# Kernel tuning notes

Measured on AMD Instinct MI355X. Metric: run time of the kernel, lower is better.

Reference implementation:

```python
import jax, jax.numpy as jnp
import numpy as np

# UKF constants (Merwe scaled sigma points)
ALPHA, BETA, KAPPA = 1.0, 2.0, 0.0
JITTER = 1e-4
S_DIM, C_DIM, M_DIM, H_DIM = 8, 2, 4, 32


def setup_inputs() -> dict:
    B, T = 1024, 256
    key = jax.random.key(0)
    ks = jax.random.split(key, 11)
    inp = {
        "X0": 0.1 * jax.random.normal(ks[0], (B, S_DIM), dtype=jnp.float32),
        "u": jax.random.normal(ks[1], (B, T, C_DIM), dtype=jnp.float32),
        "y": jax.random.normal(ks[2], (B, T, M_DIM), dtype=jnp.float32),
        # learned process model f(x,u) = x + tanh([x;u] W1 + b1) W2 + b2
        "W1": 0.1 * jax.random.normal(ks[3], (S_DIM + C_DIM, H_DIM), dtype=jnp.float32),
        "b1": jnp.zeros((H_DIM,), dtype=jnp.float32),
        "W2": 0.1 * jax.random.normal(ks[4], (H_DIM, S_DIM), dtype=jnp.float32),
        "b2": jnp.zeros((S_DIM,), dtype=jnp.float32),
        # linear measurement model h(x) = Hm x
        "Hm": 0.3 * jax.random.normal(ks[5], (M_DIM, S_DIM), dtype=jnp.float32),
        # learned diagonal noise / initial covariance (softplus parameterized)
        "lq": -3.0 + 0.1 * jax.random.normal(ks[6], (S_DIM,), dtype=jnp.float32),
        "lr": -2.0 + 0.1 * jax.random.normal(ks[7], (M_DIM,), dtype=jnp.float32),
        "lp0": -1.0 + 0.1 * jax.random.normal(ks[8], (S_DIM,), dtype=jnp.float32),
    }
    return inp


def reference(X0, u, y, W1, b1, W2, b2, Hm, lq, lr, lp0):
    B, n = X0.shape
    T = u.shape[1]
    lam = ALPHA ** 2 * (n + KAPPA) - n
    c = n + lam
    Wm = jnp.concatenate([jnp.array([lam / c], dtype=X0.dtype),
                          jnp.full((2 * n,), 0.5 / c, dtype=X0.dtype)])
    Wc = Wm.at[0].add(1.0 - ALPHA ** 2 + BETA)
    I = jnp.eye(n, dtype=X0.dtype)

    Q = jnp.diag(jax.nn.softplus(lq))            # [n,n] process noise
    R = jnp.diag(jax.nn.softplus(lr))            # [m,m] measurement noise
    P0 = jnp.broadcast_to(jnp.diag(jax.nn.softplus(lp0)), (B, n, n))  # P0(X0)

    def f(pts, u_t):  # pts [B,2n+1,n], u_t [B,C]
        uu = jnp.broadcast_to(u_t[:, None, :], pts.shape[:2] + (u_t.shape[-1],))
        z = jnp.concatenate([pts, uu], axis=-1)
        return pts + jnp.tanh(z @ W1 + b1) @ W2 + b2

    def step(carry, inp_t):
        x, P = carry            # x [B,n], P [B,n,n]
        u_t, y_t = inp_t        # u at i-1, y at i
        # sigma points via Cholesky of scaled covariance
        L = jnp.linalg.cholesky(c * P + JITTER * I)
        offs = jnp.swapaxes(L, -1, -2)  # [B,n,n]: row i = i-th column of L
        pts = jnp.concatenate([x[:, None], x[:, None] + offs, x[:, None] - offs], axis=1)  # [B,2n+1,n]
        # predict
        pts_f = f(pts, u_t)
        x_pred = jnp.einsum('s,bsn->bn', Wm, pts_f)
        dx = pts_f - x_pred[:, None]
        P_pred = jnp.einsum('s,bsn,bsm->bnm', Wc, dx, dx) + Q
        P_pred = 0.5 * (P_pred + jnp.swapaxes(P_pred, -1, -2)) + JITTER * I
        # measurement update (linear h reused on propagated sigma points)
        y_pts = pts_f @ Hm.T
        y_pred = jnp.einsum('s,bsm->bm', Wm, y_pts)
        dy = y_pts - y_pred[:, None]
        Sy = jnp.einsum('s,bsi,bsj->bij', Wc, dy, dy) + R
        Sy = 0.5 * (Sy + jnp.swapaxes(Sy, -1, -2))
        Pxy = jnp.einsum('s,bsn,bsm->bnm', Wc, dx, dy)
        # K = Pxy Sy^{-1} via solve on Sy (SPD)
        K = jnp.swapaxes(jnp.linalg.solve(Sy, jnp.swapaxes(Pxy, -1, -2)), -1, -2)
        x_new = x_pred + jnp.einsum('bnm,bm->bn', K, y_t - y_pred)
        P_new = P_pred - K @ Sy @ jnp.swapaxes(K, -1, -2)
        P_new = 0.5 * (P_new + jnp.swapaxes(P_new, -1, -2)) + JITTER * I
        q_e = 0.5 * jnp.linalg.slogdet(P_pred)[1]  # [B]
        r_e = 0.5 * jnp.linalg.slogdet(Sy)[1]      # [B]
        return (x_new, P_new), (x_new, P_new, q_e, r_e)

    # steps i = 1..T-1 use u[:, i-1] and y[:, i]
    u_seq = jnp.swapaxes(u[:, :T - 1], 0, 1)  # [T-1,B,C]
    y_seq = jnp.swapaxes(y[:, 1:], 0, 1)      # [T-1,B,M]
    _, (Xs, Ps, qs, rs) = jax.lax.scan(step, (X0, P0), (u_seq, y_seq))

    X = jnp.concatenate([X0[:, None], jnp.swapaxes(Xs, 0, 1)], axis=1)        # [B,T,n]
    P = jnp.concatenate([P0[:, None], jnp.swapaxes(Ps, 0, 1)], axis=1)        # [B,T,n,n]
    zcol = jnp.zeros((X0.shape[0], 1), dtype=X0.dtype)
    q_entr = jnp.concatenate([zcol, jnp.swapaxes(qs, 0, 1)], axis=1)          # [B,T]
    r_entr = jnp.concatenate([zcol, jnp.swapaxes(rs, 0, 1)], axis=1)          # [B,T]
    return X, P, q_entr, r_entr
```

## Files before the change

kernel.cpp:

```cpp
#include <hip/hip_runtime.h>
#include <math.h>

#define B_LEN 1024
#define T_LEN 256
#define HST 36

__device__ __forceinline__ float fast_rcp(float x) { return __builtin_amdgcn_rcpf(x); }
__device__ __forceinline__ float fast_rsq(float x) { return __builtin_amdgcn_rsqf(x); }
__device__ __forceinline__ float lane_bcast(float v, int l) {
    return __int_as_float(__builtin_amdgcn_readlane(__float_as_int(v), l));
}
__device__ __forceinline__ float fast_tanh(float x) {
    float e = __expf(2.0f * x);
    return 1.0f - 2.0f * fast_rcp(e + 1.0f);
}
__device__ __forceinline__ float softplus_f(float x) {
    return (x > 20.0f) ? x : log1pf(expf(x));
}

__global__ __launch_bounds__(128, 2)
void ukf_kernel(const float* __restrict__ X0, const float* __restrict__ U,
                const float* __restrict__ Y,  const float* __restrict__ W1,
                const float* __restrict__ B1, const float* __restrict__ W2,
                const float* __restrict__ B2, const float* __restrict__ HM,
                const float* __restrict__ LQ, const float* __restrict__ LR,
                const float* __restrict__ LP0, float* __restrict__ out)
{
    const int tid  = threadIdx.x;
    const int wid  = tid >> 6;
    const int lane = tid & 63;
    const int b    = blockIdx.x;
    const int k8   = lane & 7;
    const int g8   = lane >> 3;
    const int i8   = g8;
    const int j8   = k8;
    const int h32  = lane & 31;
    const int p2   = lane >> 5;
    const int m4   = lane & 3;
    const int sy   = lane >> 2;

    __shared__ __align__(16) float u_sh[T_LEN * 2];
    __shared__ __align__(16) float y_sh[T_LEN * 4];
    __shared__ __align__(16) float pts_sh[17 * 8];
    __shared__ __align__(16) float hid_sh[17 * HST];
    __shared__ __align__(16) float pf_sh[17 * 8];
    __shared__ __align__(16) float dx_sh[17 * 8];
    __shared__ __align__(16) float yp_sh[17 * 4];
    __shared__ __align__(16) float xp_sh[8];
    __shared__ __align__(16) float ypred_sh[4];
    __shared__ __align__(16) float Sy_sh[16];
    __shared__ __align__(16) float Pxy_sh[32];
    __shared__ __align__(16) float K_sh[32];
    __shared__ __align__(16) float Pp_sh[64];

    for (int k = tid; k < T_LEN * 2; k += 128) u_sh[k] = U[(size_t)b * (T_LEN * 2) + k];
    for (int k = tid; k < T_LEN * 4; k += 128) y_sh[k] = Y[(size_t)b * (T_LEN * 4) + k];

    float w1r[10];
    #pragma unroll
    for (int d = 0; d < 10; ++d) w1r[d] = W1[d * 32 + h32];
    const float b1r = B1[h32];
    float w2r[32];
    #pragma unroll
    for (int h = 0; h < 32; ++h) w2r[h] = W2[h * 8 + k8];
    const float b2r = B2[k8];
    float hmr[8];
    #pragma unroll
    for (int d = 0; d < 8; ++d) hmr[d] = HM[m4 * 8 + d];

    const float qdiag = softplus_f(LQ[i8]);
    const float rdiag = softplus_f(LR[m4]);

    const size_t Xbase = (size_t)b * T_LEN * 8;
    const size_t Pbase = (size_t)B_LEN * T_LEN * 8  + (size_t)b * T_LEN * 64;
    const size_t qbase = (size_t)B_LEN * T_LEN * 72 + (size_t)b * T_LEN;
    const size_t rbase = (size_t)B_LEN * T_LEN * 73 + (size_t)b * T_LEN;

    float xn[8], Pc[8];
    {
        const float4 xa = *(const float4*)&X0[b * 8];
        const float4 xb = *(const float4*)&X0[b * 8 + 4];
        xn[0] = xa.x; xn[1] = xa.y; xn[2] = xa.z; xn[3] = xa.w;
        xn[4] = xb.x; xn[5] = xb.y; xn[6] = xb.z; xn[7] = xb.w;
        const float p0k = softplus_f(LP0[k8]);
        #pragma unroll
        for (int i = 0; i < 8; ++i) Pc[i] = (i == k8) ? p0k : 0.0f;
    }
    if (wid == 0) {
        if (g8 == 0) {
            #pragma unroll
            for (int i = 0; i < 8; ++i) out[Pbase + i * 8 + k8] = Pc[i];
        }
        if (lane == 0) {
            *(float4*)&out[Xbase]     = make_float4(xn[0], xn[1], xn[2], xn[3]);
            *(float4*)&out[Xbase + 4] = make_float4(xn[4], xn[5], xn[6], xn[7]);
            out[qbase] = 0.0f; out[rbase] = 0.0f;
        }
    }

    for (int t = 1; t < T_LEN; ++t) {
        if (wid == 0) {
            float a[8];
            #pragma unroll
            for (int i = 0; i < 8; ++i) a[i] = 8.0f * Pc[i] + ((i == k8) ? 1e-4f : 0.0f);
            #pragma unroll
            for (int j = 0; j < 8; ++j) {
                const float dj  = lane_bcast(a[j], j);
                const float rv  = fast_rsq(dj);
                const float rv2 = rv * rv;
                float u[8];
                #pragma unroll
                for (int i = j + 1; i < 8; ++i) u[i] = lane_bcast(a[i], j);
                if (k8 == j) {
                    a[j] = dj * rv;
                    #pragma unroll
                    for (int i = j + 1; i < 8; ++i) a[i] *= rv;
                } else if (k8 > j) {
                    const float tt = a[j] * rv2;
                    #pragma unroll
                    for (int i = j + 1; i < 8; ++i) a[i] = fmaf(-tt, u[i], a[i]);
                }
            }
            float Lc[8];
            #pragma unroll
            for (int i = 0; i < 8; ++i) Lc[i] = (i >= k8) ? a[i] : 0.0f;
            if (g8 == 0) {
                *(float4*)&pts_sh[(1 + k8) * 8] =
                    make_float4(xn[0] + Lc[0], xn[1] + Lc[1], xn[2] + Lc[2], xn[3] + Lc[3]);
                *(float4*)&pts_sh[(1 + k8) * 8 + 4] =
                    make_float4(xn[4] + Lc[4], xn[5] + Lc[5], xn[6] + Lc[6], xn[7] + Lc[7]);
            } else if (g8 == 1) {
                *(float4*)&pts_sh[(9 + k8) * 8] =
                    make_float4(xn[0] - Lc[0], xn[1] - Lc[1], xn[2] - Lc[2], xn[3] - Lc[3]);
                *(float4*)&pts_sh[(9 + k8) * 8 + 4] =
                    make_float4(xn[4] - Lc[4], xn[5] - Lc[5], xn[6] - Lc[6], xn[7] - Lc[7]);
            } else if (g8 == 2 && k8 == 0) {
                *(float4*)&pts_sh[0] = make_float4(xn[0], xn[1], xn[2], xn[3]);
                *(float4*)&pts_sh[4] = make_float4(xn[4], xn[5], xn[6], xn[7]);
            }
        }
        __syncthreads();

        {
            const float u0 = u_sh[(t - 1) * 2 + 0];
            const float u1 = u_sh[(t - 1) * 2 + 1];
            const float ub = b1r + u0 * w1r[8] + u1 * w1r[9];
            if (wid == 0) {
                #pragma unroll
                for (int p = 0; p < 4; ++p) {
                    const int s = 2 * p + p2;
                    const float4 pa = *(const float4*)&pts_sh[s * 8];
                    const float4 pb = *(const float4*)&pts_sh[s * 8 + 4];
                    float acc = ub
                        + pa.x * w1r[0] + pa.y * w1r[1] + pa.z * w1r[2] + pa.w * w1r[3]
                        + pb.x * w1r[4] + pb.y * w1r[5] + pb.z * w1r[6] + pb.w * w1r[7];
                    hid_sh[s * HST + h32] = fast_tanh(acc);
                }
            } else {
                #pragma unroll
                for (int p = 0; p < 4; ++p) {
                    const int s = 8 + 2 * p + p2;
                    const float4 pa = *(const float4*)&pts_sh[s * 8];
                    const float4 pb = *(const float4*)&pts_sh[s * 8 + 4];
                    float acc = ub
                        + pa.x * w1r[0] + pa.y * w1r[1] + pa.z * w1r[2] + pa.w * w1r[3]
                        + pb.x * w1r[4] + pb.y * w1r[5] + pb.z * w1r[6] + pb.w * w1r[7];
                    hid_sh[s * HST + h32] = fast_tanh(acc);
                }
                if (p2 == 0) {
                    const float4 pa = *(const float4*)&pts_sh[16 * 8];
                    const float4 pb = *(const float4*)&pts_sh[16 * 8 + 4];
                    float acc = ub
                        + pa.x * w1r[0] + pa.y * w1r[1] + pa.z * w1r[2] + pa.w * w1r[3]
                        + pb.x * w1r[4] + pb.y * w1r[5] + pb.z * w1r[6] + pb.w * w1r[7];
                    hid_sh[16 * HST + h32] = fast_tanh(acc);
                }
            }
            const int srow = (wid == 0) ? g8 : (8 + g8);
            float acc = b2r;
            #pragma unroll
            for (int h = 0; h < 32; h += 4) {
                const float4 hv = *(const float4*)&hid_sh[srow * HST + h];
                acc += hv.x * w2r[h] + hv.y * w2r[h + 1] + hv.z * w2r[h + 2] + hv.w * w2r[h + 3];
            }
            pf_sh[srow * 8 + k8] = pts_sh[srow * 8 + k8] + acc;
            if (wid == 1 && lane < 8) {
                float a16 = b2r;
                #pragma unroll
                for (int h = 0; h < 32; h += 4) {
                    const float4 hv = *(const float4*)&hid_sh[16 * HST + h];
                    a16 += hv.x * w2r[h] + hv.y * w2r[h + 1] + hv.z * w2r[h + 2] + hv.w * w2r[h + 3];
                }
                pf_sh[16 * 8 + lane] = pts_sh[16 * 8 + lane] + a16;
            }
        }
        __syncthreads();

        if (wid == 0) {
            const float v0   = pf_sh[i8 * 8 + j8];
            const float v1   = pf_sh[(8 + i8) * 8 + j8];
            const float pf16 = (i8 == 0) ? pf_sh[16 * 8 + j8] : 0.0f;
            float part = ((i8 == 0) ? pf16 : v0) + v1;
            part += __shfl_xor(part, 8);
            part += __shfl_xor(part, 16);
            part += __shfl_xor(part, 32);
            const float xp = part * 0.0625f;
            if (i8 == 0) xp_sh[j8] = xp;
            dx_sh[i8 * 8 + j8]       = v0 - xp;
            dx_sh[(8 + i8) * 8 + j8] = v1 - xp;
            if (i8 == 0) dx_sh[16 * 8 + j8] = pf16 - xp;
        } else {
            float yv0, yv16 = 0.0f;
            {
                const float4 pa = *(const float4*)&pf_sh[sy * 8];
                const float4 pb = *(const float4*)&pf_sh[sy * 8 + 4];
                yv0 = pa.x * hmr[0] + pa.y * hmr[1] + pa.z * hmr[2] + pa.w * hmr[3]
                    + pb.x * hmr[4] + pb.y * hmr[5] + pb.z * hmr[6] + pb.w * hmr[7];
            }
            if (sy == 0) {
                const float4 pa = *(const float4*)&pf_sh[16 * 8];
                const float4 pb = *(const float4*)&pf_sh[16 * 8 + 4];
                yv16 = pa.x * hmr[0] + pa.y * hmr[1] + pa.z * hmr[2] + pa.w * hmr[3]
                     + pb.x * hmr[4] + pb.y * hmr[5] + pb.z * hmr[6] + pb.w * hmr[7];
            }
            float py = (sy == 0) ? yv16 : yv0;
            py += __shfl_xor(py, 4);
            py += __shfl_xor(py, 8);
            py += __shfl_xor(py, 16);
            py += __shfl_xor(py, 32);
            const float ypred = py * 0.0625f;
            if (lane < 4) ypred_sh[lane] = ypred;
            yp_sh[sy * 4 + m4] = yv0 - ypred;
            if (sy == 0) yp_sh[16 * 4 + m4] = yv16 - ypred;
        }
        __syncthreads();

        float Ppc[8];
        if (wid == 0) {
            float pp = 0.0f;
            #pragma unroll
            for (int s = 1; s < 17; ++s)
                pp += dx_sh[s * 8 + i8] * dx_sh[s * 8 + j8];
            pp *= 0.0625f;
            pp += 2.0f * dx_sh[i8] * dx_sh[j8];
            const float Ppred = pp + ((i8 == j8) ? (qdiag + 1e-4f) : 0.0f);
            Pp_sh[lane] = Ppred;
            #pragma unroll
            for (int i = 0; i < 8; ++i) Ppc[i] = Pp_sh[i * 8 + k8];
        } else {
            if (lane < 16) {
                float acc = 0.0f;
                #pragma unroll
                for (int s = 1; s < 17; ++s)
                    acc += yp_sh[s * 4 + sy] * yp_sh[s * 4 + m4];
                Sy_sh[lane] = acc * 0.0625f + 2.0f * yp_sh[sy] * yp_sh[m4]
                            + ((sy == m4) ? rdiag : 0.0f);
            } else if (lane < 48) {
                const int idx = lane - 16;
                const int ii = idx >> 2, mm = idx & 3;
                float acc = 0.0f;
                #pragma unroll
                for (int s = 1; s < 17; ++s)
                    acc += dx_sh[s * 8 + ii] * yp_sh[s * 4 + mm];
                Pxy_sh[idx] = acc * 0.0625f + 2.0f * dx_sh[ii] * yp_sh[mm];
            }
        }
        __syncthreads();

        if (wid == 0) {
            float s_[16];
            {
                const float4 r0v = *(const float4*)&Sy_sh[0];
                const float4 r1v = *(const float4*)&Sy_sh[4];
                const float4 r2v = *(const float4*)&Sy_sh[8];
                const float4 r3v = *(const float4*)&Sy_sh[12];
                s_[0]=r0v.x;  s_[1]=r0v.y;  s_[2]=r0v.z;  s_[3]=r0v.w;
                s_[4]=r1v.x;  s_[5]=r1v.y;  s_[6]=r1v.z;  s_[7]=r1v.w;
                s_[8]=r2v.x;  s_[9]=r2v.y;  s_[10]=r2v.z; s_[11]=r2v.w;
                s_[12]=r3v.x; s_[13]=r3v.y; s_[14]=r3v.z; s_[15]=r3v.w;
            }
            const float d0 = s_[0];
            const float r0 = fast_rsq(d0);
            const float L10 = s_[4] * r0, L20 = s_[8] * r0, L30 = s_[12] * r0;
            const float d1 = s_[5] - L10 * L10;
            const float r1 = fast_rsq(d1);
            const float L21 = (s_[9]  - L20 * L10) * r1;
            const float L31 = (s_[13] - L30 * L10) * r1;
            const float d2_ = s_[10] - L20 * L20 - L21 * L21;
            const float r2 = fast_rsq(d2_);
            const float L32 = (s_[14] - L30 * L20 - L31 * L21) * r2;
            const float d3 = s_[15] - L30 * L30 - L31 * L31 - L32 * L32;
            const float r3 = fast_rsq(d3);
            const float re = 0.5f * (__logf(d0) + __logf(d1) + __logf(d2_) + __logf(d3));

            const float4 pr = *(const float4*)&Pxy_sh[k8 * 4];
            const float w0_ = pr.x * r0;
            const float w1_ = (pr.y - L10 * w0_) * r1;
            const float w2_ = (pr.z - L20 * w0_ - L21 * w1_) * r2;
            const float w3_ = (pr.w - L30 * w0_ - L31 * w1_ - L32 * w2_) * r3;
            const float kk3 = w3_ * r3;
            const float kk2 = (w2_ - L32 * kk3) * r2;
            const float kk1 = (w1_ - L21 * kk2 - L31 * kk3) * r1;
            const float kk0 = (w0_ - L10 * kk1 - L20 * kk2 - L30 * kk3) * r0;
            if (g8 == 0) *(float4*)&K_sh[k8 * 4] = make_float4(kk0, kk1, kk2, kk3);

            float K_[32];
            #pragma unroll
            for (int r = 0; r < 8; ++r) {
                const float4 kr = *(const float4*)&K_sh[r * 4];
                K_[r * 4 + 0] = kr.x; K_[r * 4 + 1] = kr.y;
                K_[r * 4 + 2] = kr.z; K_[r * 4 + 3] = kr.w;
            }
            float w4[4];
            #pragma unroll
            for (int aa = 0; aa < 4; ++aa)
                w4[aa] = s_[aa * 4 + 0] * kk0 + s_[aa * 4 + 1] * kk1
                       + s_[aa * 4 + 2] * kk2 + s_[aa * 4 + 3] * kk3;
            #pragma unroll
            for (int i = 0; i < 8; ++i) {
                const float m = K_[i * 4 + 0] * w4[0] + K_[i * 4 + 1] * w4[1]
                              + K_[i * 4 + 2] * w4[2] + K_[i * 4 + 3] * w4[3];
                Pc[i] = Ppc[i] - m + ((i == k8) ? 1e-4f : 0.0f);
            }
            const float4 yt = *(const float4*)&y_sh[t * 4];
            const float4 yp = *(const float4*)&ypred_sh[0];
            const float in0 = yt.x - yp.x, in1 = yt.y - yp.y;
            const float in2 = yt.z - yp.z, in3 = yt.w - yp.w;
            const float4 xpa = *(const float4*)&xp_sh[0];
            const float4 xpb = *(const float4*)&xp_sh[4];
            float xpv[8] = {xpa.x, xpa.y, xpa.z, xpa.w, xpb.x, xpb.y, xpb.z, xpb.w};
            #pragma unroll
            for (int i = 0; i < 8; ++i)
                xn[i] = xpv[i] + K_[i * 4 + 0] * in0 + K_[i * 4 + 1] * in1
                               + K_[i * 4 + 2] * in2 + K_[i * 4 + 3] * in3;
            if (g8 == 0) {
                #pragma unroll
                for (int i = 0; i < 8; ++i)
                    out[Pbase + (size_t)t * 64 + i * 8 + k8] = Pc[i];
            }
            if (lane == 0) {
                *(float4*)&out[Xbase + (size_t)t * 8]     = make_float4(xn[0], xn[1], xn[2], xn[3]);
                *(float4*)&out[Xbase + (size_t)t * 8 + 4] = make_float4(xn[4], xn[5], xn[6], xn[7]);
                out[rbase + t] = re;
            }
        } else {
            float aq[8];
            #pragma unroll
            for (int i = 0; i < 8; ++i) aq[i] = Pp_sh[i * 8 + k8];
            float qe = 0.0f;
            #pragma unroll
            for (int j = 0; j < 8; ++j) {
                const float dj  = lane_bcast(aq[j], j);
                qe += 0.5f * __logf(dj);
                const float rv2 = fast_rcp(dj);
                float u[8];
                #pragma unroll
                for (int i = j + 1; i < 8; ++i) u[i] = lane_bcast(aq[i], j);
                if (k8 > j) {
                    const float tt = aq[j] * rv2;
                    #pragma unroll
                    for (int i = j + 1; i < 8; ++i) aq[i] = fmaf(-tt, u[i], aq[i]);
                }
            }
            if (lane == 0) out[qbase + t] = qe;
        }
    }
}

extern "C" void kernel_launch(void* const* d_in, const int* in_sizes, int n_in,
                              void* d_out, int out_size, void* d_ws, size_t ws_size,
                              hipStream_t stream) {
    (void)in_sizes; (void)n_in; (void)out_size; (void)d_ws; (void)ws_size;
    const float* X0 = (const float*)d_in[0];
    const float* U  = (const float*)d_in[1];
    const float* Y  = (const float*)d_in[2];
    const float* W1 = (const float*)d_in[3];
    const float* B1 = (const float*)d_in[4];
    const float* W2 = (const float*)d_in[5];
    const float* B2 = (const float*)d_in[6];
    const float* HM = (const float*)d_in[7];
    const float* LQ = (const float*)d_in[8];
    const float* LR = (const float*)d_in[9];
    const float* LP0 = (const float*)d_in[10];
    float* out = (float*)d_out;
    ukf_kernel<<<dim3(B_LEN), dim3(128), 0, stream>>>(X0, U, Y, W1, B1, W2, B2,
                                                      HM, LQ, LR, LP0, out);
}
```

Before: 965.6 us.

## Spread UKF step across four waves and use explicit Sy inverse for gain

Grows the block from two to four wavefronts so the sigma-point MLP evaluation is split over more waves. Wave 1 now computes Sy, its Cholesky factor and an explicit symmetrised inverse stored in shared memory, while wave 2 computes Pxy in parallel. The gain then becomes Pxy times Sy-inverse, and the covariance update uses K·Pxyᵀ in place of K·Sy·Kᵀ, which shortens the serial chain in wave 0. The cost is more threads per block, which may lower the number of independent batch blocks resident per CU, and the forming of the inverse may add slight numerical differences.

```diff
diff --git a/kernel.cpp b/kernel.cpp
--- a/kernel.cpp
+++ b/kernel.cpp
@@ -18,7 +18,7 @@
     return (x > 20.0f) ? x : log1pf(expf(x));
 }
 
-__global__ __launch_bounds__(128, 2)
+__global__ __launch_bounds__(256, 4)
 void ukf_kernel(const float* __restrict__ X0, const float* __restrict__ U,
                 const float* __restrict__ Y,  const float* __restrict__ W1,
                 const float* __restrict__ B1, const float* __restrict__ W2,
@@ -49,12 +49,13 @@
     __shared__ __align__(16) float xp_sh[8];
     __shared__ __align__(16) float ypred_sh[4];
     __shared__ __align__(16) float Sy_sh[16];
+    __shared__ __align__(16) float Si_sh[16];
     __shared__ __align__(16) float Pxy_sh[32];
     __shared__ __align__(16) float K_sh[32];
     __shared__ __align__(16) float Pp_sh[64];
 
-    for (int k = tid; k < T_LEN * 2; k += 128) u_sh[k] = U[(size_t)b * (T_LEN * 2) + k];
-    for (int k = tid; k < T_LEN * 4; k += 128) y_sh[k] = Y[(size_t)b * (T_LEN * 4) + k];
+    for (int k = tid; k < T_LEN * 2; k += 256) u_sh[k] = U[(size_t)b * (T_LEN * 2) + k];
+    for (int k = tid; k < T_LEN * 4; k += 256) y_sh[k] = Y[(size_t)b * (T_LEN * 4) + k];
 
     float w1r[10];
     #pragma unroll
@@ -145,53 +146,34 @@
             const float u0 = u_sh[(t - 1) * 2 + 0];
             const float u1 = u_sh[(t - 1) * 2 + 1];
             const float ub = b1r + u0 * w1r[8] + u1 * w1r[9];
-            if (wid == 0) {
-                #pragma unroll
-                for (int p = 0; p < 4; ++p) {
-                    const int s = 2 * p + p2;
-                    const float4 pa = *(const float4*)&pts_sh[s * 8];
-                    const float4 pb = *(const float4*)&pts_sh[s * 8 + 4];
-                    float acc = ub
-                        + pa.x * w1r[0] + pa.y * w1r[1] + pa.z * w1r[2] + pa.w * w1r[3]
-                        + pb.x * w1r[4] + pb.y * w1r[5] + pb.z * w1r[6] + pb.w * w1r[7];
-                    hid_sh[s * HST + h32] = fast_tanh(acc);
+            #pragma unroll
+            for (int p = 0; p < 2; ++p) {
+                const int s = 4 * wid + 2 * p + p2;
+                const float4 pa = *(const float4*)&pts_sh[s * 8];
+                const float4 pb = *(const float4*)&pts_sh[s * 8 + 4];
+                float acc = ub
+                    + pa.x * w1r[0] + pa.y * w1r[1] + pa.z * w1r[2] + pa.w * w1r[3]
+                    + pb.x * w1r[4] + pb.y * w1r[5] + pb.z * w1r[6] + pb.w * w1r[7];
+                hid_sh[s * HST + h32] = fast_tanh(acc);
+            }
+            if (wid == 3 && p2 == 0) {
+                const float4 pa = *(const float4*)&pts_sh[16 * 8];
+                const float4 pb = *(const float4*)&pts_sh[16 * 8 + 4];
+                float acc = ub
+                    + pa.x * w1r[0] + pa.y * w1r[1] + pa.z * w1r[2] + pa.w * w1r[3]
+                    + pb.x * w1r[4] + pb.y * w1r[5] + pb.z * w1r[6] + pb.w * w1r[7];
+                hid_sh[16 * HST + h32] = fast_tanh(acc);
+            }
+            const int nrow = (wid == 3) ? 40 : 32;
+            if (lane < nrow) {
+                const int s = ((wid == 3) ? 12 : 4 * wid) + (lane >> 3);
+                float acc = b2r;
+                #pragma unroll
+                for (int h = 0; h < 32; h += 4) {
+                    const float4 hv = *(const float4*)&hid_sh[s * HST + h];
+                    acc += hv.x * w2r[h] + hv.y * w2r[h + 1] + hv.z * w2r[h + 2] + hv.w * w2r[h + 3];
                 }
-            } else {
-                #pragma unroll
-                for (int p = 0; p < 4; ++p) {
-                    const int s = 8 + 2 * p + p2;
-                    const float4 pa = *(const float4*)&pts_sh[s * 8];
-                    const float4 pb = *(const float4*)&pts_sh[s * 8 + 4];
-                    float acc = ub
-                        + pa.x * w1r[0] + pa.y * w1r[1] + pa.z * w1r[2] + pa.w * w1r[3]
-                        + pb.x * w1r[4] + pb.y * w1r[5] + pb.z * w1r[6] + pb.w * w1r[7];
-                    hid_sh[s * HST + h32] = fast_tanh(acc);
-                }
-                if (p2 == 0) {
-                    const float4 pa = *(const float4*)&pts_sh[16 * 8];
-                    const float4 pb = *(const float4*)&pts_sh[16 * 8 + 4];
-                    float acc = ub
-                        + pa.x * w1r[0] + pa.y * w1r[1] + pa.z * w1r[2] + pa.w * w1r[3]
-                        + pb.x * w1r[4] + pb.y * w1r[5] + pb.z * w1r[6] + pb.w * w1r[7];
-                    hid_sh[16 * HST + h32] = fast_tanh(acc);
-                }
-            }
-            const int srow = (wid == 0) ? g8 : (8 + g8);
-            float acc = b2r;
-            #pragma unroll
-            for (int h = 0; h < 32; h += 4) {
-                const float4 hv = *(const float4*)&hid_sh[srow * HST + h];
-                acc += hv.x * w2r[h] + hv.y * w2r[h + 1] + hv.z * w2r[h + 2] + hv.w * w2r[h + 3];
-            }
-            pf_sh[srow * 8 + k8] = pts_sh[srow * 8 + k8] + acc;
-            if (wid == 1 && lane < 8) {
-                float a16 = b2r;
-                #pragma unroll
-                for (int h = 0; h < 32; h += 4) {
-                    const float4 hv = *(const float4*)&hid_sh[16 * HST + h];
-                    a16 += hv.x * w2r[h] + hv.y * w2r[h + 1] + hv.z * w2r[h + 2] + hv.w * w2r[h + 3];
-                }
-                pf_sh[16 * 8 + lane] = pts_sh[16 * 8 + lane] + a16;
+                pf_sh[s * 8 + k8] = pts_sh[s * 8 + k8] + acc;
             }
         }
         __syncthreads();
@@ -209,7 +191,7 @@
             dx_sh[i8 * 8 + j8]       = v0 - xp;
             dx_sh[(8 + i8) * 8 + j8] = v1 - xp;
             if (i8 == 0) dx_sh[16 * 8 + j8] = pf16 - xp;
-        } else {
+        } else if (wid == 1) {
             float yv0, yv16 = 0.0f;
             {
                 const float4 pa = *(const float4*)&pf_sh[sy * 8];
@@ -247,7 +229,7 @@
             Pp_sh[lane] = Ppred;
             #pragma unroll
             for (int i = 0; i < 8; ++i) Ppc[i] = Pp_sh[i * 8 + k8];
-        } else {
+        } else if (wid == 1) {
             if (lane < 16) {
                 float acc = 0.0f;
                 #pragma unroll
@@ -255,19 +237,7 @@
                     acc += yp_sh[s * 4 + sy] * yp_sh[s * 4 + m4];
                 Sy_sh[lane] = acc * 0.0625f + 2.0f * yp_sh[sy] * yp_sh[m4]
                             + ((sy == m4) ? rdiag : 0.0f);
-            } else if (lane < 48) {
-                const int idx = lane - 16;
-                const int ii = idx >> 2, mm = idx & 3;
-                float acc = 0.0f;
-                #pragma unroll
-                for (int s = 1; s < 17; ++s)
-                    acc += dx_sh[s * 8 + ii] * yp_sh[s * 4 + mm];
-                Pxy_sh[idx] = acc * 0.0625f + 2.0f * dx_sh[ii] * yp_sh[mm];
-            }
-        }
-        __syncthreads();
-
-        if (wid == 0) {
+            }
             float s_[16];
             {
                 const float4 r0v = *(const float4*)&Sy_sh[0];
@@ -291,19 +261,70 @@
             const float L32 = (s_[14] - L30 * L20 - L31 * L21) * r2;
             const float d3 = s_[15] - L30 * L30 - L31 * L31 - L32 * L32;
             const float r3 = fast_rsq(d3);
-            const float re = 0.5f * (__logf(d0) + __logf(d1) + __logf(d2_) + __logf(d3));
-
+            if (lane == 0)
+                out[rbase + t] = 0.5f * (__logf(d0) + __logf(d1) + __logf(d2_) + __logf(d3));
+            float z1 = -L10 * r0 * r1;
+            float z2 = -(L20 * r0 + L21 * z1) * r2;
+            float z3 = -(L30 * r0 + L31 * z1 + L32 * z2) * r3;
+            float c03 = z3 * r3;
+            float c02 = (z2 - L32 * c03) * r2;
+            float c01 = (z1 - L21 * c02 - L31 * c03) * r1;
+            float c00 = (r0 - L10 * c01 - L20 * c02 - L30 * c03) * r0;
+            float z2b = -L21 * r1 * r2;
+            float z3b = -(L31 * r1 + L32 * z2b) * r3;
+            float c13 = z3b * r3;
+            float c12 = (z2b - L32 * c13) * r2;
+            float c11 = (r1 - L21 * c12 - L31 * c13) * r1;
+            float c10 = (-L10 * c11 - L20 * c12 - L30 * c13) * r0;
+            float z3c = -L32 * r2 * r3;
+            float c23 = z3c * r3;
+            float c22 = (r2 - L32 * c23) * r2;
+            float c21 = (-L21 * c22 - L31 * c23) * r1;
+            float c20 = (-L10 * c21 - L20 * c22 - L30 * c23) * r0;
+            float c33 = r3 * r3;
+            float c32 = (-L32 * c33) * r2;
+            float c31 = (-L21 * c32 - L31 * c33) * r1;
+            float c30 = (-L10 * c31 - L20 * c32 - L30 * c33) * r0;
+            const float s01 = 0.5f * (c01 + c10), s02 = 0.5f * (c02 + c20);
+            const float s03 = 0.5f * (c03 + c30), s12 = 0.5f * (c12 + c21);
+            const float s13 = 0.5f * (c13 + c31), s23 = 0.5f * (c23 + c32);
+            if (lane == 0) {
+                *(float4*)&Si_sh[0]  = make_float4(c00, s01, s02, s03);
+                *(float4*)&Si_sh[4]  = make_float4(s01, c11, s12, s13);
+                *(float4*)&Si_sh[8]  = make_float4(s02, s12, c22, s23);
+                *(float4*)&Si_sh[12] = make_float4(s03, s13, s23, c33);
+            }
+        } else if (wid == 2) {
+            if (lane < 32) {
+                const int ii = lane >> 2, mm = lane & 3;
+                float acc = 0.0f;
+                #pragma unroll
+                for (int s = 1; s < 17; ++s)
+                    acc += dx_sh[s * 8 + ii] * yp_sh[s * 4 + mm];
+                Pxy_sh[lane] = acc * 0.0625f + 2.0f * dx_sh[ii] * yp_sh[mm];
+            }
+        }
+        __syncthreads();
+
+        if (wid == 0) {
+            float Si[16];
+            {
+                const float4 a0 = *(const float4*)&Si_sh[0];
+                const float4 a1 = *(const float4*)&Si_sh[4];
+                const float4 a2 = *(const float4*)&Si_sh[8];
+                const float4 a3 = *(const float4*)&Si_sh[12];
+                Si[0]=a0.x;  Si[1]=a0.y;  Si[2]=a0.z;  Si[3]=a0.w;
+                Si[4]=a1.x;  Si[5]=a1.y;  Si[6]=a1.z;  Si[7]=a1.w;
+                Si[8]=a2.x;  Si[9]=a2.y;  Si[10]=a2.z; Si[11]=a2.w;
+                Si[12]=a3.x; Si[13]=a3.y; Si[14]=a3.z; Si[15]=a3.w;
+            }
             const float4 pr = *(const float4*)&Pxy_sh[k8 * 4];
-            const float w0_ = pr.x * r0;
-            const float w1_ = (pr.y - L10 * w0_) * r1;
-            const float w2_ = (pr.z - L20 * w0_ - L21 * w1_) * r2;
-            const float w3_ = (pr.w - L30 * w0_ - L31 * w1_ - L32 * w2_) * r3;
-            const float kk3 = w3_ * r3;
-            const float kk2 = (w2_ - L32 * kk3) * r2;
-            const float kk1 = (w1_ - L21 * kk2 - L31 * kk3) * r1;
-            const float kk0 = (w0_ - L10 * kk1 - L20 * kk2 - L30 * kk3) * r0;
-            if (g8 == 0) *(float4*)&K_sh[k8 * 4] = make_float4(kk0, kk1, kk2, kk3);
-
+            float kk[4];
+            #pragma unroll
+            for (int aa = 0; aa < 4; ++aa)
+                kk[aa] = pr.x * Si[0 * 4 + aa] + pr.y * Si[1 * 4 + aa]
+                       + pr.z * Si[2 * 4 + aa] + pr.w * Si[3 * 4 + aa];
+            if (g8 == 0) *(float4*)&K_sh[k8 * 4] = make_float4(kk[0], kk[1], kk[2], kk[3]);
             float K_[32];
             #pragma unroll
             for (int r = 0; r < 8; ++r) {
@@ -311,15 +332,10 @@
                 K_[r * 4 + 0] = kr.x; K_[r * 4 + 1] = kr.y;
                 K_[r * 4 + 2] = kr.z; K_[r * 4 + 3] = kr.w;
             }
-            float w4[4];
-            #pragma unroll
-            for (int aa = 0; aa < 4; ++aa)
-                w4[aa] = s_[aa * 4 + 0] * kk0 + s_[aa * 4 + 1] * kk1
-                       + s_[aa * 4 + 2] * kk2 + s_[aa * 4 + 3] * kk3;
             #pragma unroll
             for (int i = 0; i < 8; ++i) {
-                const float m = K_[i * 4 + 0] * w4[0] + K_[i * 4 + 1] * w4[1]
-                              + K_[i * 4 + 2] * w4[2] + K_[i * 4 + 3] * w4[3];
+                const float m = K_[i * 4 + 0] * pr.x + K_[i * 4 + 1] * pr.y
+                              + K_[i * 4 + 2] * pr.z + K_[i * 4 + 3] * pr.w;
                 Pc[i] = Ppc[i] - m + ((i == k8) ? 1e-4f : 0.0f);
             }
             const float4 yt = *(const float4*)&y_sh[t * 4];
@@ -328,7 +344,7 @@
             const float in2 = yt.z - yp.z, in3 = yt.w - yp.w;
             const float4 xpa = *(const float4*)&xp_sh[0];
             const float4 xpb = *(const float4*)&xp_sh[4];
-            float xpv[8] = {xpa.x, xpa.y, xpa.z, xpa.w, xpb.x, xpb.y, xpb.z, xpb.w};
+            const float xpv[8] = {xpa.x, xpa.y, xpa.z, xpa.w, xpb.x, xpb.y, xpb.z, xpb.w};
             #pragma unroll
             for (int i = 0; i < 8; ++i)
                 xn[i] = xpv[i] + K_[i * 4 + 0] * in0 + K_[i * 4 + 1] * in1
@@ -341,9 +357,8 @@
             if (lane == 0) {
                 *(float4*)&out[Xbase + (size_t)t * 8]     = make_float4(xn[0], xn[1], xn[2], xn[3]);
                 *(float4*)&out[Xbase + (size_t)t * 8 + 4] = make_float4(xn[4], xn[5], xn[6], xn[7]);
-                out[rbase + t] = re;
-            }
-        } else {
+            }
+        } else if (wid == 2) {
             float aq[8];
             #pragma unroll
             for (int i = 0; i < 8; ++i) aq[i] = Pp_sh[i * 8 + k8];
@@ -383,6 +398,6 @@
     const float* LR = (const float*)d_in[9];
     const float* LP0 = (const float*)d_in[10];
     float* out = (float*)d_out;
-    ukf_kernel<<<dim3(B_LEN), dim3(128), 0, stream>>>(X0, U, Y, W1, B1, W2, B2,
+    ukf_kernel<<<dim3(B_LEN), dim3(256), 0, stream>>>(X0, U, Y, W1, B1, W2, B2,
                                                       HM, LQ, LR, LP0, out);
 }
```

Measured after the change: 1.276 ms. +32.1%, slower.
